# Kernel optimization log

Hardware: AMD Instinct MI355X
Metric: run time of the kernel (lower is better)

## Reference

```python
import jax, jax.numpy as jnp
import numpy as np

EMBED_DIM = 4096
NUM_HEADS = 32
NUM_KV_HEADS = 8
HEAD_DIM = EMBED_DIM // NUM_HEADS          # 128
Q_PER_KV = NUM_HEADS // NUM_KV_HEADS       # 4
KV_DIM = HEAD_DIM * NUM_KV_HEADS           # 1024
ROPE_BASE = 10000.0
ROTARY_DIM = HEAD_DIM                      # rotary_emb_dim = 128 (full head)


def setup_inputs() -> dict:
    key = jax.random.key(0)
    k1, k2, k3 = jax.random.split(key, 3)
    b, s = 2, 2048
    x = jax.random.normal(k1, (b, s, EMBED_DIM), dtype=jnp.float32)
    # torch nn.Linear weight layout: (out_features, in_features); scaled init
    wqkv_w = jax.random.normal(k2, (EMBED_DIM + 2 * KV_DIM, EMBED_DIM), dtype=jnp.float32) * (EMBED_DIM ** -0.5)
    wo_w = jax.random.normal(k3, (EMBED_DIM, EMBED_DIM), dtype=jnp.float32) * (EMBED_DIM ** -0.5)
    return {"x": x, "wqkv_w": wqkv_w, "wo_w": wo_w}


def _rope_cos_sin(seqlen, dtype):
    inv_freq = 1.0 / (ROPE_BASE ** (jnp.arange(0, ROTARY_DIM, 2, dtype=jnp.float32) / ROTARY_DIM))
    t = jnp.arange(seqlen, dtype=jnp.float32)
    freqs = jnp.outer(t, inv_freq)                 # (s, d/2)
    emb = jnp.concatenate([freqs, freqs], axis=-1)  # (s, d) — HF convention
    return jnp.cos(emb).astype(dtype), jnp.sin(emb).astype(dtype)


def _rotate_half(x):
    x1, x2 = jnp.split(x, 2, axis=-1)
    return jnp.concatenate([-x2, x1], axis=-1)


def _apply_rope(x, cos, sin):
    # x: (b, s, h, d); cos/sin: (s, d)
    c = cos[None, :, None, :]
    s_ = sin[None, :, None, :]
    return x * c + _rotate_half(x) * s_


def reference(x, wqkv_w, wo_w):
    b, s, _ = x.shape
    # packed QKV projection
    qkv = jnp.einsum("bse,fe->bsf", x, wqkv_w)
    # b s (h_kv * (q_per_kv + 2) * d) -> b s h_kv (q_per_kv+2) d
    qkv = qkv.reshape(b, s, NUM_KV_HEADS, Q_PER_KV + 2, HEAD_DIM)
    q = qkv[..., :Q_PER_KV, :].reshape(b, s, NUM_HEADS, HEAD_DIM)
    k = qkv[..., -2, :]   # (b, s, h_kv, d)
    v = qkv[..., -1, :]   # (b, s, h_kv, d)

    # RoPE (HF rotate_half impl, offsets = 0)
    cos, sin = _rope_cos_sin(s, x.dtype)
    q = _apply_rope(q, cos, sin)
    k = _apply_rope(k, cos, sin)

    # GQA: expand kv heads to match q heads
    k = jnp.repeat(k, Q_PER_KV, axis=2)   # (b, s, h, d)
    v = jnp.repeat(v, Q_PER_KV, axis=2)

    scale = HEAD_DIM ** -0.5
    scores = jnp.einsum("bqhd,bkhd->bhqk", q, k) * scale
    causal_mask = jnp.tril(jnp.ones((s, s), dtype=bool))
    scores = jnp.where(causal_mask[None, None], scores, jnp.finfo(scores.dtype).min)
    probs = jax.nn.softmax(scores, axis=-1)
    context = jnp.einsum("bhqk,bkhd->bqhd", probs, v)
    context = context.reshape(b, s, EMBED_DIM)
    return jnp.einsum("bse,fe->bsf", context, wo_w)
```

## Files before the change

### kernel.cpp

```cpp
#include <hip/hip_runtime.h>
#include <hip/hip_bf16.h>
#include <stdint.h>

typedef __hip_bfloat16 bf16;
typedef short bf16x8 __attribute__((ext_vector_type(8)));
typedef float f32x4 __attribute__((ext_vector_type(4)));

#define MFMA16(a, b, c) __builtin_amdgcn_mfma_f32_16x16x32_bf16((a), (b), (c), 0, 0, 0)

__device__ __forceinline__ void gload16(const void* g, void* l) {
  __builtin_amdgcn_global_load_lds((const __attribute__((address_space(1))) void*)g,
                                   (__attribute__((address_space(3))) void*)l,
                                   16, 0, 0);
}

__device__ __forceinline__ void stv(float* p, float v) { *p = v; }
__device__ __forceinline__ void stv(bf16* p, float v) { *p = __float2bfloat16(v); }

__device__ __forceinline__ float row_max16(float v) {
  int t = __builtin_amdgcn_update_dpp(0, __float_as_int(v), 0xB1, 0xF, 0xF, true);
  v = fmaxf(v, __int_as_float(t));
  t = __builtin_amdgcn_update_dpp(0, __float_as_int(v), 0x4E, 0xF, 0xF, true);
  v = fmaxf(v, __int_as_float(t));
  t = __builtin_amdgcn_update_dpp(0, __float_as_int(v), 0x124, 0xF, 0xF, true);
  v = fmaxf(v, __int_as_float(t));
  t = __builtin_amdgcn_update_dpp(0, __float_as_int(v), 0x128, 0xF, 0xF, true);
  v = fmaxf(v, __int_as_float(t));
  return v;
}
__device__ __forceinline__ float row_sum16(float v) {
  int t = __builtin_amdgcn_update_dpp(0, __float_as_int(v), 0xB1, 0xF, 0xF, true);
  v += __int_as_float(t);
  t = __builtin_amdgcn_update_dpp(0, __float_as_int(v), 0x4E, 0xF, 0xF, true);
  v += __int_as_float(t);
  t = __builtin_amdgcn_update_dpp(0, __float_as_int(v), 0x124, 0xF, 0xF, true);
  v += __int_as_float(t);
  t = __builtin_amdgcn_update_dpp(0, __float_as_int(v), 0x128, 0xF, 0xF, true);
  v += __int_as_float(t);
  return v;
}

__global__ void cast_f32_bf16(const float* __restrict__ in, bf16* __restrict__ out,
                              long n) {
  const long stride = (long)gridDim.x * blockDim.x * 8;
  for (long i = ((long)blockIdx.x * blockDim.x + threadIdx.x) * 8; i < n; i += stride) {
    const float4 a = *(const float4*)&in[i];
    const float4 b = *(const float4*)&in[i + 4];
    bf16 t[8];
    t[0] = __float2bfloat16(a.x); t[1] = __float2bfloat16(a.y);
    t[2] = __float2bfloat16(a.z); t[3] = __float2bfloat16(a.w);
    t[4] = __float2bfloat16(b.x); t[5] = __float2bfloat16(b.y);
    t[6] = __float2bfloat16(b.z); t[7] = __float2bfloat16(b.w);
    *(bf16x8*)&out[i] = *(const bf16x8*)t;
  }
}

template <typename OutT>
__global__ __launch_bounds__(512, 2) void gemm256(const bf16* __restrict__ A,
                                                  const bf16* __restrict__ B,
                                                  OutT* __restrict__ C,
                                                  int M, int N, int K) {
  const int nbn = N >> 8;
  const int nwg = gridDim.x;
  const int wg = blockIdx.x;
  const int cpx = nwg >> 3;
  const int swz = (wg & 7) * cpx + (wg >> 3);
  const int bm = swz / nbn;
  const int bn = swz - bm * nbn;

  __shared__ bf16 As[2][256][64];
  __shared__ bf16 Bs[2][256][64];

  const int tid = threadIdx.x;
  const int wave = tid >> 6, lane = tid & 63;
  const int lo = lane & 15, hi = lane >> 4;
  const int wm = wave >> 2, wn = wave & 3;

  const bf16* Ag = A + (long)(bm * 256) * K;
  const bf16* Bg = B + (long)(bn * 256) * K;

  int srow[2], scol[2], sdst[2];
#pragma unroll
  for (int j = 0; j < 2; j++) {
    const int c = j * 512 + tid;
    const int row = c >> 3;
    srow[j] = row;
    scol[j] = ((c & 7) ^ (row & 7)) * 8;
    sdst[j] = (j * 512 + wave * 64) * 8;
  }

#define STG(G, S, kt, h)                                                      \
  {                                                                           \
    _Pragma("unroll") for (int j = 0; j < 2; j++)                             \
        gload16((G) + (long)((h)*128 + srow[j]) * K + (kt) + scol[j],         \
                (S) + (h)*8192 + sdst[j]);                                    \
  }

  f32x4 acc[8][4] = {};
  const int NT = K >> 6;

  STG(Ag, &As[0][0][0], 0, 0); STG(Ag, &As[0][0][0], 0, 1);
  STG(Bg, &Bs[0][0][0], 0, 0); STG(Bg, &Bs[0][0][0], 0, 1);
  STG(Ag, &As[1][0][0], 64, 0); STG(Ag, &As[1][0][0], 64, 1);

#pragma unroll 1
  for (int t = 0; t < NT; ++t) {
    if (t >= NT - 1) asm volatile("s_waitcnt vmcnt(0)" ::: "memory");
    else             asm volatile("s_waitcnt vmcnt(4)" ::: "memory");
    __builtin_amdgcn_s_barrier();

    const bf16* Ab = &As[t & 1][0][0];
    const bf16* Bb = &Bs[t & 1][0][0];
    bf16* SAn = &As[t & 1][0][0];
    bf16* SBn = &Bs[(t + 1) & 1][0][0];
    const int kt1 = (t + 1) * 64, kt2 = (t + 2) * 64;
    const bool s1 = (t + 1 < NT), s2 = (t + 2 < NT);
    const int c0 = (hi ^ (lo & 7)) * 8;
    const int c1 = ((4 + hi) ^ (lo & 7)) * 8;

    bf16x8 a0[4], a1[4], a2[4], a3[4], b0[4], b1[4];

#pragma unroll
    for (int m = 0; m < 4; m++) {
      const int row = (wm * 128 + m * 16 + lo) * 64;
      a0[m] = *(const bf16x8*)&Ab[row + c0];
      a1[m] = *(const bf16x8*)&Ab[row + c1];
    }
#pragma unroll
    for (int n = 0; n < 4; n++)
      b0[n] = *(const bf16x8*)&Bb[(wn * 64 + n * 16 + lo) * 64 + c0];
    if (s1) STG(Bg, SBn, kt1, 0);
    __builtin_amdgcn_s_barrier();
    asm volatile("s_waitcnt lgkmcnt(0)" ::: "memory");
    __builtin_amdgcn_sched_barrier(0);
    __builtin_amdgcn_s_setprio(1);
#pragma unroll
    for (int m = 0; m < 4; m++)
#pragma unroll
      for (int n = 0; n < 4; n++) acc[m][n] = MFMA16(a0[m], b0[n], acc[m][n]);
    __builtin_amdgcn_s_setprio(0);
    __builtin_amdgcn_s_barrier();

#pragma unroll
    for (int m = 0; m < 4; m++) {
      const int row = (wm * 128 + 64 + m * 16 + lo) * 64;
      a2[m] = *(const bf16x8*)&Ab[row + c0];
      a3[m] = *(const bf16x8*)&Ab[row + c1];
    }
    if (s1) STG(Bg, SBn, kt1, 1);
    __builtin_amdgcn_s_barrier();
    asm volatile("s_waitcnt lgkmcnt(0)" ::: "memory");
    __builtin_amdgcn_sched_barrier(0);
    __builtin_amdgcn_s_setprio(1);
#pragma unroll
    for (int m = 0; m < 4; m++)
#pragma unroll
      for (int n = 0; n < 4; n++) acc[4 + m][n] = MFMA16(a2[m], b0[n], acc[4 + m][n]);
    __builtin_amdgcn_s_setprio(0);
    __builtin_amdgcn_s_barrier();

#pragma unroll
    for (int n = 0; n < 4; n++)
      b1[n] = *(const bf16x8*)&Bb[(wn * 64 + n * 16 + lo) * 64 + c1];
    if (s2) STG(Ag, SAn, kt2, 0);
    __builtin_amdgcn_s_barrier();
    asm volatile("s_waitcnt lgkmcnt(0)" ::: "memory");
    __builtin_amdgcn_sched_barrier(0);
    __builtin_amdgcn_s_setprio(1);
#pragma unroll
    for (int m = 0; m < 4; m++)
#pragma unroll
      for (int n = 0; n < 4; n++) acc[m][n] = MFMA16(a1[m], b1[n], acc[m][n]);
    __builtin_amdgcn_s_setprio(0);
    __builtin_amdgcn_s_barrier();

    if (s2) STG(Ag, SAn, kt2, 1);
    __builtin_amdgcn_s_barrier();
    __builtin_amdgcn_s_setprio(1);
#pragma unroll
    for (int m = 0; m < 4; m++)
#pragma unroll
      for (int n = 0; n < 4; n++) acc[4 + m][n] = MFMA16(a3[m], b1[n], acc[4 + m][n]);
    __builtin_amdgcn_s_setprio(0);
  }
#undef STG

  const long crow0 = (long)bm * 256 + wm * 128;
  const long ccol0 = (long)bn * 256 + wn * 64;
#pragma unroll
  for (int m = 0; m < 8; m++)
#pragma unroll
    for (int n = 0; n < 4; n++)
#pragma unroll
      for (int r = 0; r < 4; r++)
        stv(&C[(crow0 + m * 16 + hi * 4 + r) * (long)N + ccol0 + n * 16 + lo],
            acc[m][n][r]);
}

__global__ void rope_qk(bf16* __restrict__ qkv) {
  const int row = blockIdx.x;
  const int t = row & 2047;
  const float scale = 0.08838834764831845f;
  for (int p = threadIdx.x; p < 40 * 64; p += blockDim.x) {
    const int sh = p >> 6, j = p & 63;
    const int kvh = sh / 5, slot = sh - kvh * 5;
    const long base = (long)row * 6144 + kvh * 768 + slot * 128 + j;
    const float x1 = __bfloat162float(qkv[base]);
    const float x2 = __bfloat162float(qkv[base + 64]);
    const float inv = __expf(-(float)j * 0.14391156831212787f);
    const float ang = (float)t * inv;
    const float c = cosf(ang), s = sinf(ang);
    float o1 = x1 * c - x2 * s;
    float o2 = x2 * c + x1 * s;
    if (slot < 4) { o1 *= scale; o2 *= scale; }
    qkv[base] = __float2bfloat16(o1);
    qkv[base + 64] = __float2bfloat16(o2);
  }
}

__global__ void vtrans(const bf16* __restrict__ qkv, bf16* __restrict__ Vt) {
  const int tt = blockIdx.x, dd = blockIdx.y, bk = blockIdx.z;
  const int kvh = bk & 7, b = bk >> 3;
  __shared__ bf16 tile[64][65];
  const int tx = threadIdx.x, ty = threadIdx.y;
  const bf16* src = qkv + ((long)(b * 2048 + tt * 64)) * 6144 + kvh * 768 + 640 + dd * 64;
  for (int r = ty; r < 64; r += 4) tile[r][tx] = src[(long)r * 6144 + tx];
  __syncthreads();
  bf16* dst = Vt + ((long)bk * 128 + dd * 64) * 2048 + tt * 64;
  for (int r = ty; r < 64; r += 4) dst[(long)r * 2048 + tx] = tile[tx][r];
}

__global__ __launch_bounds__(256) void attn(const bf16* __restrict__ qkv,
                                            const bf16* __restrict__ Vt,
                                            bf16* __restrict__ Ctx) {
  const int lin = blockIdx.x;
  const int c = (lin & 7) * 64 + (lin >> 3);
  const int z = c & 31;
  const int kvh = (c >> 5) & 7;
  const int b = c >> 8;

  const int tid = threadIdx.x;
  const int wave = tid >> 6;
  const int lane = tid & 63;
  const int h = kvh * 4 + wave;
  const int lo = lane & 15, hi = lane >> 4;

  const bf16* Qb = qkv + (long)b * 2048 * 6144 + kvh * 768 + wave * 128;
  const bf16* Kb = qkv + (long)b * 2048 * 6144 + kvh * 768 + 512;
  const bf16* Vb = Vt + ((long)(b * 8 + kvh)) * 128 * 2048;

  __shared__ bf16 Kl[2][32][128];
  __shared__ bf16 Vl[2][128][32];
  __shared__ bf16 Plds[4][32][40];

  int krow[2], kcol[2], vrow[2], vcol[2], sbase[2];
#pragma unroll
  for (int cl = 0; cl < 2; cl++) {
    const int t = cl * 256 + tid;
    krow[cl] = t >> 4;
    kcol[cl] = ((t & 15) ^ (krow[cl] & 15)) * 8;
    vrow[cl] = t >> 2;
    vcol[cl] = ((t & 3) ^ ((vrow[cl] >> 1) & 3)) * 8;
    sbase[cl] = cl * 2048 + wave * 512;
  }

#define STAGE_KV(bufi, k0_)                                                    \
  {                                                                            \
    _Pragma("unroll") for (int cl = 0; cl < 2; cl++)                           \
        gload16(Kb + (long)((k0_) + krow[cl]) * 6144 + kcol[cl],               \
                &Kl[bufi][0][0] + sbase[cl]);                                  \
    _Pragma("unroll") for (int cl = 0; cl < 2; cl++)                           \
        gload16(Vb + (long)vrow[cl] * 2048 + (k0_) + vcol[cl],                 \
                &Vl[bufi][0][0] + sbase[cl]);                                  \
  }

#pragma unroll 1
  for (int pass = 0; pass < 2; ++pass) {
    const int qw = pass ? 63 - z : z;
    const int q0 = qw * 32;

    bf16x8 qf[2][4];
#pragma unroll
    for (int qb = 0; qb < 2; qb++)
#pragma unroll
      for (int dc = 0; dc < 4; dc++)
        qf[qb][dc] =
            *(const bf16x8*)&Qb[(long)(q0 + qb * 16 + lo) * 6144 + dc * 32 + hi * 8];

    f32x4 acc[2][8] = {};
    float mrow[2][4], lrow[2][4];
#pragma unroll
    for (int qb = 0; qb < 2; qb++)
#pragma unroll
      for (int r = 0; r < 4; r++) {
        mrow[qb][r] = -1e30f;
        lrow[qb][r] = 0.0f;
      }

    STAGE_KV(0, 0);
    if (qw > 0) STAGE_KV(1, 32);

#pragma unroll 1
    for (int kt = 0; kt <= qw; ++kt) {
      if (kt < qw) asm volatile("s_waitcnt vmcnt(4)" ::: "memory");
      else         asm volatile("s_waitcnt vmcnt(0)" ::: "memory");
      __builtin_amdgcn_s_barrier();

      const int bi = kt & 1;
      const int k0 = kt * 32;

      f32x4 sacc[2][2] = {};
      __builtin_amdgcn_s_setprio(1);
#pragma unroll
      for (int kb = 0; kb < 2; kb++)
#pragma unroll
        for (int dc = 0; dc < 4; dc++) {
          const int row = kb * 16 + lo;
          const int p = (dc * 4 + hi) ^ (row & 15);
          const bf16x8 kf = *(const bf16x8*)&Kl[bi][row][p * 8];
          sacc[0][kb] = MFMA16(qf[0][dc], kf, sacc[0][kb]);
          sacc[1][kb] = MFMA16(qf[1][dc], kf, sacc[1][kb]);
        }
      __builtin_amdgcn_s_setprio(0);

      if (kt == qw) {
#pragma unroll
        for (int qb = 0; qb < 2; qb++)
#pragma unroll
          for (int kb = 0; kb < 2; kb++) {
            const int q = q0 + qb * 16 + hi * 4;
            const int k = k0 + kb * 16 + lo;
#pragma unroll
            for (int r = 0; r < 4; r++)
              if (k > q + r) sacc[qb][kb][r] = -1e30f;
          }
      }

      float ex = -1.0f;
#pragma unroll
      for (int qb = 0; qb < 2; qb++)
#pragma unroll
        for (int kb = 0; kb < 2; kb++)
#pragma unroll
          for (int r = 0; r < 4; r++)
            ex = fmaxf(ex, sacc[qb][kb][r] - mrow[qb][r]);

      if (!__all(ex <= 0.0f)) {
        float sf[2][4];
#pragma unroll
        for (int qb = 0; qb < 2; qb++)
#pragma unroll
          for (int r = 0; r < 4; r++) {
            const float pm = row_max16(fmaxf(sacc[qb][0][r], sacc[qb][1][r]));
            const float mn = fmaxf(mrow[qb][r], pm);
            sf[qb][r] = __expf(mrow[qb][r] - mn);
            mrow[qb][r] = mn;
            lrow[qb][r] *= sf[qb][r];
          }
#pragma unroll
        for (int qb = 0; qb < 2; qb++)
#pragma unroll
          for (int dt = 0; dt < 8; dt++)
#pragma unroll
            for (int r = 0; r < 4; r++) acc[qb][dt][r] *= sf[qb][r];
      }

#pragma unroll
      for (int qb = 0; qb < 2; qb++)
#pragma unroll
        for (int r = 0; r < 4; r++) {
          float p0 = __expf(sacc[qb][0][r] - mrow[qb][r]);
          float p1 = __expf(sacc[qb][1][r] - mrow[qb][r]);
          lrow[qb][r] += row_sum16(p0 + p1);
          Plds[wave][qb * 16 + hi * 4 + r][lo] = __float2bfloat16(p0);
          Plds[wave][qb * 16 + hi * 4 + r][16 + lo] = __float2bfloat16(p1);
        }

      bf16x8 pa[2];
#pragma unroll
      for (int qb = 0; qb < 2; qb++)
        pa[qb] = *(const bf16x8*)&Plds[wave][qb * 16 + lo][hi * 8];

      __builtin_amdgcn_s_setprio(1);
#pragma unroll
      for (int dt = 0; dt < 8; dt++) {
        const int row = dt * 16 + lo;
        const int p = hi ^ ((row >> 1) & 3);
        const bf16x8 vf = *(const bf16x8*)&Vl[bi][row][p * 8];
        acc[0][dt] = MFMA16(pa[0], vf, acc[0][dt]);
        acc[1][dt] = MFMA16(pa[1], vf, acc[1][dt]);
      }
      __builtin_amdgcn_s_setprio(0);

      asm volatile("s_waitcnt lgkmcnt(0)" ::: "memory");
      __builtin_amdgcn_s_barrier();
      if (kt + 2 <= qw) STAGE_KV(bi, (kt + 2) * 32);
    }

#pragma unroll
    for (int qb = 0; qb < 2; qb++)
#pragma unroll
      for (int r = 0; r < 4; r++) {
        const float rl = 1.0f / lrow[qb][r];
#pragma unroll
        for (int dt = 0; dt < 8; dt++) {
          const float o = acc[qb][dt][r] * rl;
          const long row = (long)b * 2048 + q0 + qb * 16 + hi * 4 + r;
          Ctx[row * 4096 + h * 128 + dt * 16 + lo] = __float2bfloat16(o);
        }
      }
  }
#undef STAGE_KV
}


extern "C" void kernel_launch(void* const* d_in, const int* in_sizes, int n_in,
                              void* d_out, int out_size, void* d_ws, size_t ws_size,
                              hipStream_t stream) {
  (void)in_sizes; (void)n_in; (void)out_size; (void)ws_size;
  const float* x = (const float*)d_in[0];
  const float* wqkv = (const float*)d_in[1];
  const float* wo = (const float*)d_in[2];
  float* out = (float*)d_out;

  const long NX = 4096L * 4096;
  const long NW1 = 6144L * 4096;

  const size_t XB_B = (size_t)NX * 2;
  const size_t WQ_B = (size_t)NW1 * 2;
  const size_t QKV_B = WQ_B;

  char* w = (char*)d_ws;
  bf16* xb = (bf16*)w;
  bf16* wqkvb = (bf16*)(w + XB_B);
  bf16* qkvp = (bf16*)(w + XB_B + WQ_B);
  bf16* Vtp = (bf16*)(w + XB_B + WQ_B + QKV_B);
  bf16* wob = xb;
  bf16* ctx = wqkvb;

  cast_f32_bf16<<<2048, 256, 0, stream>>>(x, xb, NX);
  cast_f32_bf16<<<2048, 256, 0, stream>>>(wqkv, wqkvb, NW1);

  gemm256<bf16><<<16 * 24, 512, 0, stream>>>(xb, wqkvb, qkvp, 4096, 6144, 4096);

  rope_qk<<<4096, 256, 0, stream>>>(qkvp);
  vtrans<<<dim3(32, 2, 16), dim3(64, 4), 0, stream>>>(qkvp, Vtp);

  cast_f32_bf16<<<2048, 256, 0, stream>>>(wo, wob, NX);

  attn<<<dim3(512), 256, 0, stream>>>(qkvp, Vtp, ctx);

  gemm256<float><<<16 * 16, 512, 0, stream>>>(ctx, wob, out, 4096, 4096, 4096);
}
```

Baseline: 645.4 us.

## Double the attention key tile to 64 keys per pipeline iteration

The flash-attention loop now stages and processes 64 keys per iteration instead of 32. Loads are widened to four 16-byte chunks per thread for K and V, and the V swizzle is changed to fit the wider tile. The P·V product is split into two 32-key sub-steps that reuse the existing P staging buffer. This halves the number of barriers, waitcnts and loop iterations per query tile, which cuts synchronization overhead. In exchange, LDS use per block doubles, which can lower occupancy, and the diagonal tile does some extra masked work.

```diff
diff --git a/kernel.cpp b/kernel.cpp
--- a/kernel.cpp
+++ b/kernel.cpp
@@ -249,35 +249,31 @@
   const bf16* Kb = qkv + (long)b * 2048 * 6144 + kvh * 768 + 512;
   const bf16* Vb = Vt + ((long)(b * 8 + kvh)) * 128 * 2048;
 
-  __shared__ bf16 Kl[2][32][128];
-  __shared__ bf16 Vl[2][128][32];
+  __shared__ bf16 Kl[2][64][128];
+  __shared__ bf16 Vl[2][128][64];
   __shared__ bf16 Plds[4][32][40];
 
-  int krow[2], kcol[2], vrow[2], vcol[2], sbase[2];
-#pragma unroll
-  for (int cl = 0; cl < 2; cl++) {
-    const int t = cl * 256 + tid;
-    krow[cl] = t >> 4;
-    kcol[cl] = ((t & 15) ^ (krow[cl] & 15)) * 8;
-    vrow[cl] = t >> 2;
-    vcol[cl] = ((t & 3) ^ ((vrow[cl] >> 1) & 3)) * 8;
-    sbase[cl] = cl * 2048 + wave * 512;
-  }
+  const int kr0 = tid >> 4;
+  const int kc = ((tid & 15) ^ (kr0 & 15)) * 8;
+  const int vr0 = tid >> 3;
+  const int vc = ((tid & 7) ^ (vr0 & 7)) * 8;
+  const int wbase = wave * 512;
 
 #define STAGE_KV(bufi, k0_)                                                    \
   {                                                                            \
-    _Pragma("unroll") for (int cl = 0; cl < 2; cl++)                           \
-        gload16(Kb + (long)((k0_) + krow[cl]) * 6144 + kcol[cl],               \
-                &Kl[bufi][0][0] + sbase[cl]);                                  \
-    _Pragma("unroll") for (int cl = 0; cl < 2; cl++)                           \
-        gload16(Vb + (long)vrow[cl] * 2048 + (k0_) + vcol[cl],                 \
-                &Vl[bufi][0][0] + sbase[cl]);                                  \
+    _Pragma("unroll") for (int cl = 0; cl < 4; cl++)                           \
+        gload16(Kb + (long)((k0_) + cl * 16 + kr0) * 6144 + kc,                \
+                &Kl[bufi][0][0] + cl * 2048 + wbase);                          \
+    _Pragma("unroll") for (int cl = 0; cl < 4; cl++)                           \
+        gload16(Vb + (long)(cl * 32 + vr0) * 2048 + (k0_) + vc,                \
+                &Vl[bufi][0][0] + cl * 2048 + wbase);                          \
   }
 
 #pragma unroll 1
   for (int pass = 0; pass < 2; ++pass) {
     const int qw = pass ? 63 - z : z;
     const int q0 = qw * 32;
+    const int nkt = (qw >> 1) + 1;
 
     bf16x8 qf[2][4];
 #pragma unroll
@@ -298,36 +294,36 @@
       }
 
     STAGE_KV(0, 0);
-    if (qw > 0) STAGE_KV(1, 32);
+    if (nkt > 1) STAGE_KV(1, 64);
 
 #pragma unroll 1
-    for (int kt = 0; kt <= qw; ++kt) {
-      if (kt < qw) asm volatile("s_waitcnt vmcnt(4)" ::: "memory");
-      else         asm volatile("s_waitcnt vmcnt(0)" ::: "memory");
+    for (int kt = 0; kt < nkt; ++kt) {
+      if (kt < nkt - 1) asm volatile("s_waitcnt vmcnt(8)" ::: "memory");
+      else              asm volatile("s_waitcnt vmcnt(0)" ::: "memory");
       __builtin_amdgcn_s_barrier();
 
       const int bi = kt & 1;
-      const int k0 = kt * 32;
-
-      f32x4 sacc[2][2] = {};
+      const int k0 = kt * 64;
+
+      f32x4 sacc[2][4] = {};
       __builtin_amdgcn_s_setprio(1);
 #pragma unroll
-      for (int kb = 0; kb < 2; kb++)
+      for (int kb = 0; kb < 4; kb++)
 #pragma unroll
         for (int dc = 0; dc < 4; dc++) {
           const int row = kb * 16 + lo;
-          const int p = (dc * 4 + hi) ^ (row & 15);
+          const int p = (dc * 4 + hi) ^ lo;
           const bf16x8 kf = *(const bf16x8*)&Kl[bi][row][p * 8];
           sacc[0][kb] = MFMA16(qf[0][dc], kf, sacc[0][kb]);
           sacc[1][kb] = MFMA16(qf[1][dc], kf, sacc[1][kb]);
         }
       __builtin_amdgcn_s_setprio(0);
 
-      if (kt == qw) {
+      if (kt == nkt - 1) {
 #pragma unroll
         for (int qb = 0; qb < 2; qb++)
 #pragma unroll
-          for (int kb = 0; kb < 2; kb++) {
+          for (int kb = 0; kb < 4; kb++) {
             const int q = q0 + qb * 16 + hi * 4;
             const int k = k0 + kb * 16 + lo;
 #pragma unroll
@@ -340,7 +336,7 @@
 #pragma unroll
       for (int qb = 0; qb < 2; qb++)
 #pragma unroll
-        for (int kb = 0; kb < 2; kb++)
+        for (int kb = 0; kb < 4; kb++)
 #pragma unroll
           for (int r = 0; r < 4; r++)
             ex = fmaxf(ex, sacc[qb][kb][r] - mrow[qb][r]);
@@ -351,7 +347,9 @@
         for (int qb = 0; qb < 2; qb++)
 #pragma unroll
           for (int r = 0; r < 4; r++) {
-            const float pm = row_max16(fmaxf(sacc[qb][0][r], sacc[qb][1][r]));
+            const float pm = row_max16(
+                fmaxf(fmaxf(sacc[qb][0][r], sacc[qb][1][r]),
+                      fmaxf(sacc[qb][2][r], sacc[qb][3][r])));
             const float mn = fmaxf(mrow[qb][r], pm);
             sf[qb][r] = __expf(mrow[qb][r] - mn);
             mrow[qb][r] = mn;
@@ -369,32 +367,47 @@
       for (int qb = 0; qb < 2; qb++)
 #pragma unroll
         for (int r = 0; r < 4; r++) {
-          float p0 = __expf(sacc[qb][0][r] - mrow[qb][r]);
-          float p1 = __expf(sacc[qb][1][r] - mrow[qb][r]);
-          lrow[qb][r] += row_sum16(p0 + p1);
-          Plds[wave][qb * 16 + hi * 4 + r][lo] = __float2bfloat16(p0);
-          Plds[wave][qb * 16 + hi * 4 + r][16 + lo] = __float2bfloat16(p1);
+          float s0 = __expf(sacc[qb][0][r] - mrow[qb][r]);
+          float s1 = __expf(sacc[qb][1][r] - mrow[qb][r]);
+          float s2 = __expf(sacc[qb][2][r] - mrow[qb][r]);
+          float s3 = __expf(sacc[qb][3][r] - mrow[qb][r]);
+          sacc[qb][0][r] = s0; sacc[qb][1][r] = s1;
+          sacc[qb][2][r] = s2; sacc[qb][3][r] = s3;
+          lrow[qb][r] += row_sum16((s0 + s1) + (s2 + s3));
         }
 
-      bf16x8 pa[2];
-#pragma unroll
-      for (int qb = 0; qb < 2; qb++)
-        pa[qb] = *(const bf16x8*)&Plds[wave][qb * 16 + lo][hi * 8];
-
-      __builtin_amdgcn_s_setprio(1);
-#pragma unroll
-      for (int dt = 0; dt < 8; dt++) {
-        const int row = dt * 16 + lo;
-        const int p = hi ^ ((row >> 1) & 3);
-        const bf16x8 vf = *(const bf16x8*)&Vl[bi][row][p * 8];
-        acc[0][dt] = MFMA16(pa[0], vf, acc[0][dt]);
-        acc[1][dt] = MFMA16(pa[1], vf, acc[1][dt]);
+#pragma unroll
+      for (int ks = 0; ks < 2; ks++) {
+#pragma unroll
+        for (int qb = 0; qb < 2; qb++)
+#pragma unroll
+          for (int r = 0; r < 4; r++) {
+            Plds[wave][qb * 16 + hi * 4 + r][lo] =
+                __float2bfloat16(sacc[qb][ks * 2][r]);
+            Plds[wave][qb * 16 + hi * 4 + r][16 + lo] =
+                __float2bfloat16(sacc[qb][ks * 2 + 1][r]);
+          }
+
+        bf16x8 pa[2];
+#pragma unroll
+        for (int qb = 0; qb < 2; qb++)
+          pa[qb] = *(const bf16x8*)&Plds[wave][qb * 16 + lo][hi * 8];
+
+        __builtin_amdgcn_s_setprio(1);
+#pragma unroll
+        for (int dt = 0; dt < 8; dt++) {
+          const int row = dt * 16 + lo;
+          const int p = (ks * 4 + hi) ^ (row & 7);
+          const bf16x8 vf = *(const bf16x8*)&Vl[bi][row][p * 8];
+          acc[0][dt] = MFMA16(pa[0], vf, acc[0][dt]);
+          acc[1][dt] = MFMA16(pa[1], vf, acc[1][dt]);
+        }
+        __builtin_amdgcn_s_setprio(0);
       }
-      __builtin_amdgcn_s_setprio(0);
 
       asm volatile("s_waitcnt lgkmcnt(0)" ::: "memory");
       __builtin_amdgcn_s_barrier();
-      if (kt + 2 <= qw) STAGE_KV(bi, (kt + 2) * 32);
+      if (kt + 2 < nkt) STAGE_KV(bi, (kt + 2) * 64);
     }
 
 #pragma unroll
```

Result: faster. 589.2 us (-8.7%).
